# Optimization experiments

Hardware: AMD Instinct MI355X
Metric: run time of the kernel (lower is better)

Reference implementation:

```python
import jax, jax.numpy as jnp
import numpy as np

N_SPECIES = 4
NUM_MODELS = 8
LAYER_DIMS = [384, 160, 128, 96, 1]
CELU_ALPHA = 0.1
N_ATOMS = 50000  # divisible by N_SPECIES -> balanced routing


def setup_inputs() -> dict:
    key = jax.random.key(0)
    ks = jax.random.split(key, 2 + 2 * (len(LAYER_DIMS) - 1))
    # Balanced species assignment: exactly N_ATOMS/N_SPECIES atoms per species,
    # randomly permuted (mirrors a real molecule's scattered per-species atoms
    # while keeping per-species group sizes static for jit).
    base = jnp.tile(jnp.arange(N_SPECIES, dtype=jnp.int64), N_ATOMS // N_SPECIES)
    species = jax.random.permutation(ks[0], base)[None, :]  # [1, N_ATOMS]
    aev = jax.random.normal(ks[1], (1, N_ATOMS, LAYER_DIMS[0]), dtype=jnp.float32)
    inp = {"species": species, "aev": aev}
    # Fused ensemble params per species: W [S, M, in, out], b [S, M, 1, out]
    for li in range(len(LAYER_DIMS) - 1):
        fin, fout = LAYER_DIMS[li], LAYER_DIMS[li + 1]
        scale = 1.0 / np.sqrt(fin)
        inp[f"W{li+1}"] = jax.random.uniform(
            ks[2 + 2 * li], (N_SPECIES, NUM_MODELS, fin, fout),
            dtype=jnp.float32, minval=-scale, maxval=scale)
        inp[f"b{li+1}"] = jax.random.uniform(
            ks[3 + 2 * li], (N_SPECIES, NUM_MODELS, 1, fout),
            dtype=jnp.float32, minval=-scale, maxval=scale)
    return inp


def _ensemble_mlp(x, W1, b1, W2, b2, W3, b3, W4, b4):
    # x: [S, n, F] routed atoms per species; W: [S, M, fin, fout]; b: [S, M, 1, fout]
    celu = lambda h: jax.nn.celu(h, alpha=CELU_ALPHA)
    h = celu(jnp.einsum('snf,smfo->smno', x, W1) + b1)   # [S, M, n, 160]
    h = celu(jnp.einsum('smnf,smfo->smno', h, W2) + b2)  # [S, M, n, 128]
    h = celu(jnp.einsum('smnf,smfo->smno', h, W3) + b3)  # [S, M, n, 96]
    h = jnp.einsum('smnf,smfo->smno', h, W4) + b4        # [S, M, n, 1]
    return h.mean(axis=1)                                 # mean over models -> [S, n, 1]


def reference(species, aev, W1, b1, W2, b2, W3, b3, W4, b4):
    n_atoms = species.shape[1]
    n_per = n_atoms // N_SPECIES
    # species-routed gather: stable argsort groups atoms by species; counts are
    # static (balanced) so reshape into [S, n_per] groups (== per-species index_select)
    order = jnp.argsort(species.reshape(-1), stable=True)
    x = aev.reshape(n_atoms, -1)[order].reshape(N_SPECIES, n_per, -1)
    atom_e = _ensemble_mlp(x, W1, b1, W2, b2, W3, b3, W4, b4)  # [S, n_per, 1]
    mol_energies = jnp.sum(atom_e).reshape(1)  # scatter-sum over all atoms/species
    return mol_energies
```

## Files before the change

### kernel.cpp

```cpp
#include <hip/hip_runtime.h>


#define NSP 4
#define NMODELS 8
#define MSPLIT 2
#define MPB (NMODELS / MSPLIT)
#define NATOMS 50000
#define NPER (NATOMS / NSP)
#define NPAD 12544
#define D0 384
#define D1 160
#define D2 128
#define D3 96
#define NRBLK ((NATOMS + 255) / 256)
#define ABLK 128
#define BPS ((NPER + ABLK - 1) / ABLK)
#define FRAGS_SM 184
#define CHUNKS_M 23
#define TOT_CHUNKS (MPB * CHUNKS_M)

typedef float f32x4 __attribute__((ext_vector_type(4)));
typedef __bf16 bf16x8 __attribute__((ext_vector_type(8)));

#define MFMA16(a, b, c) __builtin_amdgcn_mfma_f32_16x16x32_bf16((a), (b), (c), 0, 0, 0)

#define PALL_BYTES ((size_t)NSP * NMODELS * FRAGS_SM * 1024)
#define PBIAS_OFF PALL_BYTES
#define PBIAS_BYTES ((size_t)NSP * NMODELS * 512 * 2)
#define ORDER_OFF (PBIAS_OFF + PBIAS_BYTES)
#define BCNT_OFF (ORDER_OFF + (size_t)NATOMS * 4)
#define BPFX_OFF (BCNT_OFF + (size_t)NRBLK * NSP * 4)
#define BASE_OFF (BPFX_OFF + (size_t)NRBLK * NSP * 4)
#define AEVB_OFF (BASE_OFF + 1024)
#define AEVB_BYTES ((size_t)NSP * NPAD * D0 * 2)

static __device__ __forceinline__ unsigned short bfbits(float f) {
  __bf16 h = (__bf16)f;
  return __builtin_bit_cast(unsigned short, h);
}

static __device__ __forceinline__ float celu01(float x) {
  return fmaxf(x, 0.f) + 0.1f * fminf(0.f, __expf(x * 10.f) - 1.f);
}

static __device__ __forceinline__ void gload16(const void* g, void* l) {
  __builtin_amdgcn_global_load_lds(
      (const __attribute__((address_space(1))) unsigned int*)g,
      (__attribute__((address_space(3))) unsigned int*)l, 16, 0, 0);
}

__global__ __launch_bounds__(256) void count_kernel(const int* __restrict__ species,
                                                    int* __restrict__ bcnt) {
  __shared__ int cnt[NSP];
  int t = threadIdx.x;
  if (t < NSP) cnt[t] = 0;
  __syncthreads();
  int i = blockIdx.x * 256 + t;
  if (i < NATOMS) atomicAdd(&cnt[species[i]], 1);
  __syncthreads();
  if (t < NSP) bcnt[blockIdx.x * NSP + t] = cnt[t];
}

__global__ __launch_bounds__(256) void scan_kernel(const int* __restrict__ bcnt,
                                                   int* __restrict__ bpfx,
                                                   int* __restrict__ base) {
  int w = threadIdx.x >> 6;
  int lane = threadIdx.x & 63;
  __shared__ int totals[NSP];
  int carry = 0;
  for (int c = 0; c < (NRBLK + 63) / 64; ++c) {
    int idx = c * 64 + lane;
    int v = (idx < NRBLK) ? bcnt[idx * NSP + w] : 0;
    int incl = v;
    for (int off = 1; off < 64; off <<= 1) {
      int tv = __shfl_up(incl, off);
      if (lane >= off) incl += tv;
    }
    if (idx < NRBLK) bpfx[idx * NSP + w] = carry + incl - v;
    carry += __shfl(incl, 63);
  }
  if (lane == 0) totals[w] = carry;
  __syncthreads();
  if (threadIdx.x == 0) {
    int run = 0;
    for (int s = 0; s < NSP; ++s) { base[s] = run; run += totals[s]; }
  }
}

__global__ __launch_bounds__(256) void route_kernel(const int* __restrict__ species,
                                                    const int* __restrict__ bpfx,
                                                    const int* __restrict__ base,
                                                    int* __restrict__ order) {
  __shared__ int sp[256];
  int t = threadIdx.x;
  int i = blockIdx.x * 256 + t;
  sp[t] = (i < NATOMS) ? species[i] : -1;
  __syncthreads();
  if (i < NATOMS) {
    int s = sp[t];
    int rank = 0;
    for (int j = 0; j < t; ++j) rank += (sp[j] == s) ? 1 : 0;
    order[base[s] + bpfx[blockIdx.x * NSP + s] + rank] = i;
  }
}

__global__ __launch_bounds__(256) void aev_pack(const float* __restrict__ aev,
                                                const int* __restrict__ order,
                                                unsigned short* __restrict__ aevb) {
  int tid = blockIdx.x * 256 + threadIdx.x;
  const int perRow = D0 / 8;
  int row = tid / perRow;
  int seg = tid - row * perRow;
  if (row >= NSP * NPAD) return;
  int s = row / NPAD;
  int slot = row - s * NPAD;
  unsigned short o[8];
  if (slot < NPER) {
    int src = order[s * NPER + slot];
    const float4* q = (const float4*)(aev + (size_t)src * D0 + seg * 8);
    float4 v0 = q[0], v1 = q[1];
    o[0] = bfbits(v0.x); o[1] = bfbits(v0.y); o[2] = bfbits(v0.z); o[3] = bfbits(v0.w);
    o[4] = bfbits(v1.x); o[5] = bfbits(v1.y); o[6] = bfbits(v1.z); o[7] = bfbits(v1.w);
  } else {
#pragma unroll
    for (int e = 0; e < 8; ++e) o[e] = 0;
  }
  *(int4*)(aevb + (size_t)row * D0 + seg * 8) = *(const int4*)o;
}

__global__ __launch_bounds__(256) void pack_kernel(const float* __restrict__ W,
                                                   unsigned* __restrict__ dst,
                                                   int K, int N, int NT, int fragBase,
                                                   int total) {
  int tid = blockIdx.x * 256 + threadIdx.x;
  if (tid >= total) return;
  int per_sm = K * N / 2;
  int smi = tid / per_sm;
  int rem = tid - smi * per_sm;
  int frag = rem >> 8;
  int wi = rem & 255;
  int l = wi >> 2, d = wi & 3;
  int kf = frag / NT;
  int nt = frag - kf * NT;
  int k = kf * 32 + ((l >> 4) << 3) + 2 * d;
  int n = nt * 16 + (l & 15);
  const float* p = W + ((size_t)smi * K + k) * N + n;
  unsigned lo = bfbits(p[0]);
  unsigned hi = bfbits(p[N]);
  dst[((size_t)smi * FRAGS_SM + fragBase + frag) * 256 + wi] = lo | (hi << 16);
}

__global__ __launch_bounds__(256) void param_pack(const float* __restrict__ b1,
                                                  const float* __restrict__ b2,
                                                  const float* __restrict__ b3,
                                                  const float* __restrict__ W4,
                                                  const float* __restrict__ b4,
                                                  unsigned short* __restrict__ dst) {
  int i = blockIdx.x * 256 + threadIdx.x;
  if (i >= NSP * NMODELS * 512) return;
  int smi = i >> 9, o = i & 511;
  unsigned short v = 0;
  if (o < 160) v = bfbits(b1[smi * 160 + o]);
  else if (o < 288) v = bfbits(b2[smi * 128 + (o - 160)]);
  else if (o < 384) v = bfbits(b3[smi * 96 + (o - 288)]);
  else if (o < 480) v = bfbits(W4[smi * 96 + (o - 384)]);
  else if (o < 482) {
    unsigned u = __builtin_bit_cast(unsigned, b4[smi]);
    v = (unsigned short)((o == 480) ? (u & 0xffffu) : (u >> 16));
  }
  dst[i] = v;
}

#define STAGE2(gn)                                                       \
  do {                                                                   \
    if ((gn) < TOT_CHUNKS) {                                             \
      const char* _s = wsrc + (size_t)(gn) * 8192;                       \
      char* _d = (char*)stage + (size_t)((gn) & 3) * 8192 + w * 2048;    \
      gload16(_s, _d);                                                   \
      gload16(_s + 1024, _d + 1024);                                     \
    }                                                                    \
  } while (0)

#define PAIR_HEAD()                                                      \
  do {                                                                   \
    asm volatile("s_waitcnt vmcnt(0)" ::: "memory");                     \
    __builtin_amdgcn_s_barrier();                                        \
    STAGE2(gc + 2);                                                      \
    STAGE2(gc + 3);                                                      \
  } while (0)

#define CHUNK_END() rb_off = (rb_off + 8192u) & 32767u; ++gc

__global__ __launch_bounds__(256, 2) void mlp_kernel(
    const unsigned short* __restrict__ aevb,
    const unsigned short* __restrict__ pAll, const unsigned short* __restrict__ pPar,
    float* __restrict__ out) {
  __shared__ alignas(16) unsigned short stage[4][4096];
  __shared__ alignas(16) __bf16 hbuf[4][32][168];
  __shared__ alignas(16) unsigned short hpar[MPB * 512];

  const int nwg = NSP * BPS * MSPLIT;
  const int cpx = nwg / 8;
  const int blk = (blockIdx.x % 8) * cpx + blockIdx.x / 8;
  const int s = blk / (BPS * MSPLIT);
  const int rem = blk - s * (BPS * MSPLIT);
  const int mh = rem / BPS;
  const int sb = rem - mh * BPS;
  const int tid = threadIdx.x;
  const int w = tid >> 6;
  const int l = tid & 63;
  const int l15 = l & 15;
  const int l4 = l >> 4;

  {
    const int4* src = (const int4*)(pPar + ((size_t)(s * NMODELS + mh * MPB)) * 512);
    ((int4*)hpar)[tid] = src[tid];
  }

  const size_t smBase = (size_t)(s * NMODELS + mh * MPB) * FRAGS_SM;
  const char* wsrc = (const char*)pAll + smBase * 1024 + (size_t)w * 2048 + (size_t)l * 16;

  bf16x8 a1[2][12];
#pragma unroll
  for (int mt = 0; mt < 2; ++mt) {
    int row = s * NPAD + sb * ABLK + w * 32 + mt * 16 + l15;
    const bf16x8* rp = (const bf16x8*)(aevb + (size_t)row * D0 + l4 * 8);
#pragma unroll
    for (int kf = 0; kf < 12; ++kf) a1[mt][kf] = rp[kf * 4];
  }

  const __bf16* hb = (const __bf16*)hpar;
  float acc4[2][4] = {{0.f, 0.f, 0.f, 0.f}, {0.f, 0.f, 0.f, 0.f}};
  float bbacc = 0.f;

  __syncthreads();

  STAGE2(0);
  STAGE2(1);

  int gc = 0;
  unsigned rb_off = 0;

#pragma unroll 1
  for (int m = 0; m < MPB; ++m) {
    const int par = m & 1;
    f32x4 C[2][10];

#pragma unroll
    for (int mt = 0; mt < 2; ++mt)
#pragma unroll
      for (int nt = 0; nt < 10; ++nt) {
        f32x4 z; z[0] = z[1] = z[2] = z[3] = 0.f; C[mt][nt] = z;
      }
#pragma unroll
    for (int c = 0; c < 15; ++c) {
      if ((c & 1) == par) PAIR_HEAD();
      const bf16x8* sbuf = (const bf16x8*)((const char*)stage + rb_off);
#pragma unroll
      for (int j = 0; j < 8; ++j) {
        const int f = c * 8 + j;
        bf16x8 b = sbuf[j * 64 + l];
        C[0][f % 10] = MFMA16(a1[0][f / 10], b, C[0][f % 10]);
        C[1][f % 10] = MFMA16(a1[1][f / 10], b, C[1][f % 10]);
      }
      CHUNK_END();
    }
#pragma unroll
    for (int nt = 0; nt < 10; ++nt) {
      float bias = (float)hb[m * 512 + nt * 16 + l15];
#pragma unroll
      for (int mt = 0; mt < 2; ++mt)
#pragma unroll
        for (int r = 0; r < 4; ++r)
          hbuf[w][mt * 16 + l4 * 4 + r][nt * 16 + l15] = (__bf16)celu01(C[mt][nt][r] + bias);
    }

    bf16x8 a2[2][5];
#pragma unroll
    for (int mt = 0; mt < 2; ++mt)
#pragma unroll
      for (int kf = 0; kf < 5; ++kf)
        a2[mt][kf] = *(const bf16x8*)&hbuf[w][mt * 16 + l15][kf * 32 + l4 * 8];

#pragma unroll
    for (int mt = 0; mt < 2; ++mt)
#pragma unroll
      for (int nt = 0; nt < 8; ++nt) {
        f32x4 z; z[0] = z[1] = z[2] = z[3] = 0.f; C[mt][nt] = z;
      }
#pragma unroll
    for (int lc = 0; lc < 5; ++lc) {
      if (((15 + lc) & 1) == par) PAIR_HEAD();
      const bf16x8* sbuf = (const bf16x8*)((const char*)stage + rb_off);
#pragma unroll
      for (int j = 0; j < 8; ++j) {
        bf16x8 b = sbuf[j * 64 + l];
        C[0][j] = MFMA16(a2[0][lc], b, C[0][j]);
        C[1][j] = MFMA16(a2[1][lc], b, C[1][j]);
      }
      CHUNK_END();
    }
#pragma unroll
    for (int nt = 0; nt < 8; ++nt) {
      float bias = (float)hb[m * 512 + 160 + nt * 16 + l15];
#pragma unroll
      for (int mt = 0; mt < 2; ++mt)
#pragma unroll
        for (int r = 0; r < 4; ++r)
          hbuf[w][mt * 16 + l4 * 4 + r][nt * 16 + l15] = (__bf16)celu01(C[mt][nt][r] + bias);
    }

    bf16x8 a3[2][4];
#pragma unroll
    for (int mt = 0; mt < 2; ++mt)
#pragma unroll
      for (int kf = 0; kf < 4; ++kf)
        a3[mt][kf] = *(const bf16x8*)&hbuf[w][mt * 16 + l15][kf * 32 + l4 * 8];

#pragma unroll
    for (int mt = 0; mt < 2; ++mt)
#pragma unroll
      for (int nt = 0; nt < 6; ++nt) {
        f32x4 z; z[0] = z[1] = z[2] = z[3] = 0.f; C[mt][nt] = z;
      }
#pragma unroll
    for (int lc = 0; lc < 3; ++lc) {
      if (((20 + lc) & 1) == par) PAIR_HEAD();
      const bf16x8* sbuf = (const bf16x8*)((const char*)stage + rb_off);
#pragma unroll
      for (int j = 0; j < 8; ++j) {
        const int f = lc * 8 + j;
        bf16x8 b = sbuf[j * 64 + l];
        C[0][f % 6] = MFMA16(a3[0][f / 6], b, C[0][f % 6]);
        C[1][f % 6] = MFMA16(a3[1][f / 6], b, C[1][f % 6]);
      }
      CHUNK_END();
    }

    float e[2][4] = {{0.f, 0.f, 0.f, 0.f}, {0.f, 0.f, 0.f, 0.f}};
#pragma unroll
    for (int nt = 0; nt < 6; ++nt) {
      float b3v = (float)hb[m * 512 + 288 + nt * 16 + l15];
      float w4v = (float)hb[m * 512 + 384 + nt * 16 + l15];
#pragma unroll
      for (int mt = 0; mt < 2; ++mt)
#pragma unroll
        for (int r = 0; r < 4; ++r)
          e[mt][r] += celu01(C[mt][nt][r] + b3v) * w4v;
    }
#pragma unroll
    for (int mt = 0; mt < 2; ++mt)
#pragma unroll
      for (int r = 0; r < 4; ++r) acc4[mt][r] += e[mt][r];
    bbacc += ((const float*)hpar)[m * 256 + 240];
  }

  asm volatile("s_waitcnt vmcnt(0)" ::: "memory");

  float tot = 0.f;
#pragma unroll
  for (int mt = 0; mt < 2; ++mt)
#pragma unroll
    for (int r = 0; r < 4; ++r) {
      float v = acc4[mt][r];
      v += __shfl_xor(v, 1);
      v += __shfl_xor(v, 2);
      v += __shfl_xor(v, 4);
      v += __shfl_xor(v, 8);
      int slot = sb * ABLK + w * 32 + mt * 16 + l4 * 4 + r;
      if (l15 == 0 && slot < NPER) tot += v + bbacc;
    }
  tot *= (1.f / NMODELS);
#pragma unroll
  for (int off = 1; off < 64; off <<= 1) tot += __shfl_xor(tot, off);
  if (l == 0) atomicAdd(out, tot);
}

extern "C" void kernel_launch(void* const* d_in, const int* in_sizes, int n_in,
                              void* d_out, int out_size, void* d_ws, size_t ws_size,
                              hipStream_t stream) {
  (void)in_sizes; (void)n_in; (void)out_size; (void)ws_size;
  const int* species = (const int*)d_in[0];
  const float* aev = (const float*)d_in[1];
  const float* W1 = (const float*)d_in[2];
  const float* b1 = (const float*)d_in[3];
  const float* W2 = (const float*)d_in[4];
  const float* b2 = (const float*)d_in[5];
  const float* W3 = (const float*)d_in[6];
  const float* b3 = (const float*)d_in[7];
  const float* W4 = (const float*)d_in[8];
  const float* b4 = (const float*)d_in[9];
  float* out = (float*)d_out;
  char* ws = (char*)d_ws;

  unsigned short* pAll = (unsigned short*)ws;
  unsigned short* pPar = (unsigned short*)(ws + PBIAS_OFF);
  int* order = (int*)(ws + ORDER_OFF);
  int* bcnt = (int*)(ws + BCNT_OFF);
  int* bpfx = (int*)(ws + BPFX_OFF);
  int* base = (int*)(ws + BASE_OFF);
  unsigned short* aevb = (unsigned short*)(ws + AEVB_OFF);

  hipMemsetAsync(d_out, 0, sizeof(float), stream);

  count_kernel<<<NRBLK, 256, 0, stream>>>(species, bcnt);
  scan_kernel<<<1, 256, 0, stream>>>(bcnt, bpfx, base);
  route_kernel<<<NRBLK, 256, 0, stream>>>(species, bpfx, base, order);

  {
    int total = NSP * NPAD * (D0 / 8);
    aev_pack<<<total / 256, 256, 0, stream>>>(aev, order, aevb);
  }
  {
    int total = NSP * NMODELS * D0 * D1 / 2;
    pack_kernel<<<(total + 255) / 256, 256, 0, stream>>>(W1, (unsigned*)pAll, D0, D1, D1 / 16, 0, total);
  }
  {
    int total = NSP * NMODELS * D1 * D2 / 2;
    pack_kernel<<<(total + 255) / 256, 256, 0, stream>>>(W2, (unsigned*)pAll, D1, D2, D2 / 16, 120, total);
  }
  {
    int total = NSP * NMODELS * D2 * D3 / 2;
    pack_kernel<<<(total + 255) / 256, 256, 0, stream>>>(W3, (unsigned*)pAll, D2, D3, D3 / 16, 160, total);
  }
  {
    int total = NSP * NMODELS * 512;
    param_pack<<<(total + 255) / 256, 256, 0, stream>>>(b1, b2, b3, W4, b4, pPar);
  }

  mlp_kernel<<<NSP * BPS * MSPLIT, 256, 0, stream>>>(aevb, pAll, pPar, out);
}
```

Measured before the change: 214.7 us.

## Replace static grid with persistent work-stealing over atom-block/model units

The MLP kernel becomes persistent: 512 workgroups pull (atom block, model) units from a global atomic counter. The aev fragments are reloaded only when the group changes. The 4-deep weight staging with pair barriers is replaced by 2-deep double buffering with a barrier per chunk. Bias reads now go to global memory instead of an LDS copy, and one atomicAdd is issued per unit. The goal is better load balance and tail behaviour. The cost is more barriers, a shallower prefetch, and many more atomics.

```diff
diff --git a/kernel.cpp b/kernel.cpp
--- a/kernel.cpp
+++ b/kernel.cpp
@@ -3,8 +3,6 @@
 
 #define NSP 4
 #define NMODELS 8
-#define MSPLIT 2
-#define MPB (NMODELS / MSPLIT)
 #define NATOMS 50000
 #define NPER (NATOMS / NSP)
 #define NPAD 12544
@@ -16,8 +14,9 @@
 #define ABLK 128
 #define BPS ((NPER + ABLK - 1) / ABLK)
 #define FRAGS_SM 184
-#define CHUNKS_M 23
-#define TOT_CHUNKS (MPB * CHUNKS_M)
+#define NGROUP (NSP * BPS)
+#define NUNIT (NGROUP * NMODELS)
+#define NWORK 512
 
 typedef float f32x4 __attribute__((ext_vector_type(4)));
 typedef __bf16 bf16x8 __attribute__((ext_vector_type(8)));
@@ -33,6 +32,7 @@
 #define BASE_OFF (BPFX_OFF + (size_t)NRBLK * NSP * 4)
 #define AEVB_OFF (BASE_OFF + 1024)
 #define AEVB_BYTES ((size_t)NSP * NPAD * D0 * 2)
+#define CTR_OFF (AEVB_OFF + AEVB_BYTES)
 
 static __device__ __forceinline__ unsigned short bfbits(float f) {
   __bf16 h = (__bf16)f;
@@ -171,79 +171,59 @@
   dst[i] = v;
 }
 
-#define STAGE2(gn)                                                       \
-  do {                                                                   \
-    if ((gn) < TOT_CHUNKS) {                                             \
-      const char* _s = wsrc + (size_t)(gn) * 8192;                       \
-      char* _d = (char*)stage + (size_t)((gn) & 3) * 8192 + w * 2048;    \
-      gload16(_s, _d);                                                   \
-      gload16(_s + 1024, _d + 1024);                                     \
-    }                                                                    \
-  } while (0)
-
-#define PAIR_HEAD()                                                      \
-  do {                                                                   \
-    asm volatile("s_waitcnt vmcnt(0)" ::: "memory");                     \
-    __builtin_amdgcn_s_barrier();                                        \
-    STAGE2(gc + 2);                                                      \
-    STAGE2(gc + 3);                                                      \
-  } while (0)
-
-#define CHUNK_END() rb_off = (rb_off + 8192u) & 32767u; ++gc
-
 __global__ __launch_bounds__(256, 2) void mlp_kernel(
     const unsigned short* __restrict__ aevb,
     const unsigned short* __restrict__ pAll, const unsigned short* __restrict__ pPar,
-    float* __restrict__ out) {
-  __shared__ alignas(16) unsigned short stage[4][4096];
+    int* __restrict__ uctr, float* __restrict__ out) {
+  __shared__ alignas(16) unsigned short stage[2][4096];
   __shared__ alignas(16) __bf16 hbuf[4][32][168];
-  __shared__ alignas(16) unsigned short hpar[MPB * 512];
-
-  const int nwg = NSP * BPS * MSPLIT;
-  const int cpx = nwg / 8;
-  const int blk = (blockIdx.x % 8) * cpx + blockIdx.x / 8;
-  const int s = blk / (BPS * MSPLIT);
-  const int rem = blk - s * (BPS * MSPLIT);
-  const int mh = rem / BPS;
-  const int sb = rem - mh * BPS;
+  __shared__ int ush;
+
   const int tid = threadIdx.x;
   const int w = tid >> 6;
   const int l = tid & 63;
   const int l15 = l & 15;
   const int l4 = l >> 4;
 
-  {
-    const int4* src = (const int4*)(pPar + ((size_t)(s * NMODELS + mh * MPB)) * 512);
-    ((int4*)hpar)[tid] = src[tid];
-  }
-
-  const size_t smBase = (size_t)(s * NMODELS + mh * MPB) * FRAGS_SM;
-  const char* wsrc = (const char*)pAll + smBase * 1024 + (size_t)w * 2048 + (size_t)l * 16;
-
   bf16x8 a1[2][12];
-#pragma unroll
-  for (int mt = 0; mt < 2; ++mt) {
-    int row = s * NPAD + sb * ABLK + w * 32 + mt * 16 + l15;
-    const bf16x8* rp = (const bf16x8*)(aevb + (size_t)row * D0 + l4 * 8);
-#pragma unroll
-    for (int kf = 0; kf < 12; ++kf) a1[mt][kf] = rp[kf * 4];
-  }
-
-  const __bf16* hb = (const __bf16*)hpar;
-  float acc4[2][4] = {{0.f, 0.f, 0.f, 0.f}, {0.f, 0.f, 0.f, 0.f}};
-  float bbacc = 0.f;
-
-  __syncthreads();
-
-  STAGE2(0);
-  STAGE2(1);
-
-  int gc = 0;
-  unsigned rb_off = 0;
-
-#pragma unroll 1
-  for (int m = 0; m < MPB; ++m) {
-    const int par = m & 1;
+  int cur_g = -1;
+
+  while (true) {
+    if (tid == 0) ush = atomicAdd(uctr, 1);
+    __syncthreads();
+    const int u = ush;
+    if (u >= NUNIT) break;
+    const int g = u >> 3;
+    const int m = u & 7;
+    const int s = g / BPS;
+    const int sb = g - s * BPS;
+
+    if (g != cur_g) {
+      cur_g = g;
+#pragma unroll
+      for (int mt = 0; mt < 2; ++mt) {
+        int row = s * NPAD + sb * ABLK + w * 32 + mt * 16 + l15;
+        const bf16x8* rp = (const bf16x8*)(aevb + (size_t)row * D0 + l4 * 8);
+#pragma unroll
+        for (int kf = 0; kf < 12; ++kf) a1[mt][kf] = rp[kf * 4];
+      }
+    }
+
+    const int smi = s * NMODELS + m;
+    const char* wu = (const char*)pAll + (size_t)smi * FRAGS_SM * 1024 +
+                     (size_t)w * 2048 + (size_t)l * 16;
+    const unsigned short* pb = pPar + (size_t)smi * 512;
+
+    auto stg = [&](int c) {
+      char* d = (char*)stage + (c & 1) * 8192 + w * 2048;
+      const char* sp = wu + (size_t)c * 8192;
+      gload16(sp, d);
+      gload16(sp + 1024, d + 1024);
+    };
+
+    stg(0);
+    __syncthreads();
+
     f32x4 C[2][10];
 
 #pragma unroll
@@ -254,8 +234,8 @@
       }
 #pragma unroll
     for (int c = 0; c < 15; ++c) {
-      if ((c & 1) == par) PAIR_HEAD();
-      const bf16x8* sbuf = (const bf16x8*)((const char*)stage + rb_off);
+      stg(c + 1);
+      const bf16x8* sbuf = (const bf16x8*)((const char*)stage + (c & 1) * 8192);
 #pragma unroll
       for (int j = 0; j < 8; ++j) {
         const int f = c * 8 + j;
@@ -263,11 +243,11 @@
         C[0][f % 10] = MFMA16(a1[0][f / 10], b, C[0][f % 10]);
         C[1][f % 10] = MFMA16(a1[1][f / 10], b, C[1][f % 10]);
       }
-      CHUNK_END();
+      __syncthreads();
     }
 #pragma unroll
     for (int nt = 0; nt < 10; ++nt) {
-      float bias = (float)hb[m * 512 + nt * 16 + l15];
+      float bias = (float)__builtin_bit_cast(__bf16, pb[nt * 16 + l15]);
 #pragma unroll
       for (int mt = 0; mt < 2; ++mt)
 #pragma unroll
@@ -290,19 +270,20 @@
       }
 #pragma unroll
     for (int lc = 0; lc < 5; ++lc) {
-      if (((15 + lc) & 1) == par) PAIR_HEAD();
-      const bf16x8* sbuf = (const bf16x8*)((const char*)stage + rb_off);
+      const int c = 15 + lc;
+      stg(c + 1);
+      const bf16x8* sbuf = (const bf16x8*)((const char*)stage + (c & 1) * 8192);
 #pragma unroll
       for (int j = 0; j < 8; ++j) {
         bf16x8 b = sbuf[j * 64 + l];
         C[0][j] = MFMA16(a2[0][lc], b, C[0][j]);
         C[1][j] = MFMA16(a2[1][lc], b, C[1][j]);
       }
-      CHUNK_END();
+      __syncthreads();
     }
 #pragma unroll
     for (int nt = 0; nt < 8; ++nt) {
-      float bias = (float)hb[m * 512 + 160 + nt * 16 + l15];
+      float bias = (float)__builtin_bit_cast(__bf16, pb[160 + nt * 16 + l15]);
 #pragma unroll
       for (int mt = 0; mt < 2; ++mt)
 #pragma unroll
@@ -325,8 +306,9 @@
       }
 #pragma unroll
     for (int lc = 0; lc < 3; ++lc) {
-      if (((20 + lc) & 1) == par) PAIR_HEAD();
-      const bf16x8* sbuf = (const bf16x8*)((const char*)stage + rb_off);
+      const int c = 20 + lc;
+      if (c + 1 < 23) stg(c + 1);
+      const bf16x8* sbuf = (const bf16x8*)((const char*)stage + (c & 1) * 8192);
 #pragma unroll
       for (int j = 0; j < 8; ++j) {
         const int f = lc * 8 + j;
@@ -334,46 +316,39 @@
         C[0][f % 6] = MFMA16(a3[0][f / 6], b, C[0][f % 6]);
         C[1][f % 6] = MFMA16(a3[1][f / 6], b, C[1][f % 6]);
       }
-      CHUNK_END();
+      __syncthreads();
     }
 
     float e[2][4] = {{0.f, 0.f, 0.f, 0.f}, {0.f, 0.f, 0.f, 0.f}};
 #pragma unroll
     for (int nt = 0; nt < 6; ++nt) {
-      float b3v = (float)hb[m * 512 + 288 + nt * 16 + l15];
-      float w4v = (float)hb[m * 512 + 384 + nt * 16 + l15];
+      float b3v = (float)__builtin_bit_cast(__bf16, pb[288 + nt * 16 + l15]);
+      float w4v = (float)__builtin_bit_cast(__bf16, pb[384 + nt * 16 + l15]);
 #pragma unroll
       for (int mt = 0; mt < 2; ++mt)
 #pragma unroll
         for (int r = 0; r < 4; ++r)
           e[mt][r] += celu01(C[mt][nt][r] + b3v) * w4v;
     }
-#pragma unroll
-    for (int mt = 0; mt < 2; ++mt)
-#pragma unroll
-      for (int r = 0; r < 4; ++r) acc4[mt][r] += e[mt][r];
-    bbacc += ((const float*)hpar)[m * 256 + 240];
-  }
-
-  asm volatile("s_waitcnt vmcnt(0)" ::: "memory");
-
-  float tot = 0.f;
-#pragma unroll
-  for (int mt = 0; mt < 2; ++mt)
-#pragma unroll
-    for (int r = 0; r < 4; ++r) {
-      float v = acc4[mt][r];
-      v += __shfl_xor(v, 1);
-      v += __shfl_xor(v, 2);
-      v += __shfl_xor(v, 4);
-      v += __shfl_xor(v, 8);
-      int slot = sb * ABLK + w * 32 + mt * 16 + l4 * 4 + r;
-      if (l15 == 0 && slot < NPER) tot += v + bbacc;
-    }
-  tot *= (1.f / NMODELS);
-#pragma unroll
-  for (int off = 1; off < 64; off <<= 1) tot += __shfl_xor(tot, off);
-  if (l == 0) atomicAdd(out, tot);
+    float b4v = ((const float*)pPar)[(size_t)smi * 256 + 240];
+    float tot = 0.f;
+#pragma unroll
+    for (int mt = 0; mt < 2; ++mt)
+#pragma unroll
+      for (int r = 0; r < 4; ++r) {
+        float v = e[mt][r];
+        v += __shfl_xor(v, 1);
+        v += __shfl_xor(v, 2);
+        v += __shfl_xor(v, 4);
+        v += __shfl_xor(v, 8);
+        int slot = sb * ABLK + w * 32 + mt * 16 + l4 * 4 + r;
+        if (l15 == 0 && slot < NPER) tot += v + b4v;
+      }
+    tot *= (1.f / NMODELS);
+#pragma unroll
+    for (int off = 1; off < 64; off <<= 1) tot += __shfl_xor(tot, off);
+    if (l == 0) atomicAdd(out, tot);
+  }
 }
 
 extern "C" void kernel_launch(void* const* d_in, const int* in_sizes, int n_in,
@@ -400,8 +375,10 @@
   int* bpfx = (int*)(ws + BPFX_OFF);
   int* base = (int*)(ws + BASE_OFF);
   unsigned short* aevb = (unsigned short*)(ws + AEVB_OFF);
+  int* uctr = (int*)(ws + CTR_OFF);
 
   hipMemsetAsync(d_out, 0, sizeof(float), stream);
+  hipMemsetAsync(uctr, 0, sizeof(int), stream);
 
   count_kernel<<<NRBLK, 256, 0, stream>>>(species, bcnt);
   scan_kernel<<<1, 256, 0, stream>>>(bcnt, bpfx, base);
@@ -428,5 +405,5 @@
     param_pack<<<(total + 255) / 256, 256, 0, stream>>>(b1, b2, b3, W4, b4, pPar);
   }
 
-  mlp_kernel<<<NSP * BPS * MSPLIT, 256, 0, stream>>>(aevb, pAll, pPar, out);
-}
+  mlp_kernel<<<NWORK, 256, 0, stream>>>(aevb, pAll, pPar, uctr, out);
+}
```

After: 271.6 us. 26.5% more time.
